# Kernel tuning notes

Hardware: AMD Instinct MI355X
Metric: run time of the kernel (lower is better)

The kernel has to match this reference:

```python
import jax, jax.numpy as jnp
import numpy as np

V, E, H = 50000, 256, 256   # vocab, emb_dim, hid_dim
R, S, W = 64, 32, 64        # reviews, sentences/review, words/sentence
UF = 20                     # user feature dim


def _bigru_last(x, wih, whh, bih, bhh):
    """Bidirectional GRU over x [B,T,D]; returns sum of final hidden states of
    the two directions, shape [B,H]. Params stacked over direction axis 0."""
    Hh = whh.shape[-1]

    def onedir(xd, wi, wh, bi, bh):
        gx = jnp.einsum('btd,gd->btg', xd, wi) + bi  # [B,T,3H] input gates precomputed

        def step(h, gxt):
            gh = h @ wh.T + bh
            r = jax.nn.sigmoid(gxt[:, :Hh] + gh[:, :Hh])
            z = jax.nn.sigmoid(gxt[:, Hh:2 * Hh] + gh[:, Hh:2 * Hh])
            n = jnp.tanh(gxt[:, 2 * Hh:] + r * gh[:, 2 * Hh:])
            return (1.0 - z) * n + z * h, None

        h0 = jnp.zeros((xd.shape[0], Hh), xd.dtype)
        hT, _ = jax.lax.scan(step, h0, jnp.swapaxes(gx, 0, 1))
        return hT

    return (onedir(x, wih[0], whh[0], bih[0], bhh[0])
            + onedir(x[:, ::-1], wih[1], whh[1], bih[1], bhh[1]))


def setup_inputs() -> dict:
    key = jax.random.key(0)
    ks = iter(jax.random.split(key, 40))

    def wmat(shape, scale=0.05):
        return jax.random.normal(next(ks), shape, jnp.float32) * scale

    inp = {}
    inp['inputs'] = jax.random.randint(next(ks), (R, S, W), 0, V)
    inp['sent_lengths'] = jax.random.randint(next(ks), (R, S), 1, W)
    inp['sent_counts'] = jax.random.randint(next(ks), (R,), 1, S)
    inp['user_feats'] = jax.random.normal(next(ks), (R, UF), jnp.float32)
    inp['embed'] = wmat((V, E))
    for name, din in (('wg', E), ('sg', H), ('rg', H + UF)):
        inp[name + '_wih'] = wmat((2, 3 * H, din))
        inp[name + '_whh'] = wmat((2, 3 * H, H))
        inp[name + '_bih'] = jnp.zeros((2, 3 * H), jnp.float32)
        inp[name + '_bhh'] = jnp.zeros((2, 3 * H), jnp.float32)
    inp['rfc_w1'] = wmat((H // 2, H + UF)); inp['rfc_b1'] = jnp.zeros((H // 2,), jnp.float32)
    inp['rfc_w2'] = wmat((1, H // 2));      inp['rfc_b2'] = jnp.zeros((1,), jnp.float32)
    inp['pfc_w1'] = wmat((H // 2, H));      inp['pfc_b1'] = jnp.zeros((H // 2,), jnp.float32)
    inp['pfc_w2'] = wmat((9, H // 2));      inp['pfc_b2'] = jnp.zeros((9,), jnp.float32)
    inp['uf_w'] = jnp.ones((UF,), jnp.float32)  # user_feats_weights
    return inp


def reference(inputs, sent_lengths, sent_counts, user_feats, embed,
              wg_wih, wg_whh, wg_bih, wg_bhh,
              sg_wih, sg_whh, sg_bih, sg_bhh,
              rg_wih, rg_whh, rg_bih, rg_bhh,
              rfc_w1, rfc_b1, rfc_w2, rfc_b2,
              pfc_w1, pfc_b1, pfc_w2, pfc_b2, uf_w):
    Rr, Sr, Wr = inputs.shape
    emb = embed[inputs]  # [R,S,W,E]  (dropout = identity in eval mode)
    # word-level bi-GRU, all R*S sentences batched together
    sent = _bigru_last(emb.reshape(Rr * Sr, Wr, emb.shape[-1]),
                       wg_wih, wg_whh, wg_bih, wg_bhh).reshape(Rr, Sr, -1)
    # sentence-level bi-GRU, batch over reviews
    rev = _bigru_last(sent, sg_wih, sg_whh, sg_bih, sg_bhh)  # [R,H]
    # F.normalize(user_feats) * user_feats_weights
    nrm = jnp.maximum(jnp.linalg.norm(user_feats, axis=-1, keepdims=True), 1e-12)
    p_batch = jnp.concatenate([rev, (user_feats / nrm) * uf_w], axis=-1)  # [R,H+20]
    r_stars = (jax.nn.selu(p_batch @ rfc_w1.T + rfc_b1) @ rfc_w2.T + rfc_b2)[:, 0]  # [R]
    # review-level bi-GRU over the sequence of reviews (batch 1)
    doc = _bigru_last(p_batch[None], rg_wih, rg_whh, rg_bih, rg_bhh)[0]  # [H]
    p_stars = jax.nn.selu(doc @ pfc_w1.T + pfc_b1) @ pfc_w2.T + pfc_b2  # [9]
    return p_stars, r_stars
```

## Files before the change

kernel.cpp:

```cpp
#include <hip/hip_runtime.h>
#include <math.h>

#define R_ 64
#define S_ 32
#define W_ 64
#define H_ 256
#define UF_ 20
#define TC 4

typedef short bf16x8 __attribute__((ext_vector_type(8)));
typedef float f32x4  __attribute__((ext_vector_type(4)));

#define MFMA(a,b,c) __builtin_amdgcn_mfma_f32_16x16x32_bf16((a),(b),(c),0,0,0)

typedef const unsigned int __attribute__((address_space(1)))* gp_t;
typedef unsigned int __attribute__((address_space(3)))* lp_t;
#define GLOAD16(SRC, DST) \
  __builtin_amdgcn_global_load_lds((gp_t)(const void*)(SRC), (lp_t)(void*)(DST), 16, 0, 0)

#define SW(r) ((((r)>>1)&7)<<3)

#define BFRAG(ff) ((ff) < 40 ? Breg[(ff) < 40 ? (ff) : 0] \
                 : *(const bf16x8*)&Bl[w][(ff) >= 40 ? (ff)-40 : 0][l*8])

__device__ __forceinline__ float sigf(float x){ return 1.0f/(1.0f+__expf(-x)); }
__device__ __forceinline__ float tanhf_(float x){ float e=__expf(2.0f*x); return 1.0f-2.0f/(e+1.0f); }
__device__ __forceinline__ float seluf_(float x){
  const float sc=1.0507009873554805f, al=1.6732632423543772f;
  return x>0.0f ? sc*x : sc*al*(expf(x)-1.0f);
}
__device__ __forceinline__ short tobf(float f){
  unsigned u=__float_as_uint(f); u += 0x7fffu + ((u>>16)&1u); return (short)(u>>16);
}
__device__ __forceinline__ float bf2f(short s){
  return __uint_as_float(((unsigned)(unsigned short)s) << 16);
}
__device__ __forceinline__ unsigned pk2(float a, float b){
  return (unsigned)(unsigned short)tobf(a) | ((unsigned)(unsigned short)tobf(b) << 16);
}

__global__ void prep_word_w(const float* __restrict__ wih, const float* __restrict__ whh,
                            short* __restrict__ Bw)
{
  int idx = blockIdx.x*256 + threadIdx.x;
  int lane = idx & 63;
  int rest = idx >> 6;
  int f  = rest % 6;  rest /= 6;
  int kt = rest % 16; rest /= 16;
  int w  = rest % 8;
  int d  = rest / 8;
  int gate = f >> 1;
  int j = 32*w + (f&1)*16 + (lane&15);
  int row = gate*256 + j;
  const float* W = (kt < 8 ? wih : whh) + (size_t)d*768*256;
  int k = (kt&7)*32 + (lane>>4)*8;
  short* dst = Bw + ((((size_t)(d*8 + w)*16 + kt)*6 + f)*64 + lane)*8;
#pragma unroll
  for (int jj=0;jj<8;jj++) dst[jj] = tobf(W[(size_t)row*256 + k + jj]);
}

__global__ void prep_rnn_w(const float* __restrict__ whh, short* __restrict__ Bs)
{
  int idx = blockIdx.x*256 + threadIdx.x;
  int lane = idx & 63;
  int rest = idx >> 6;
  int f  = rest % 6; rest /= 6;
  int kt = rest % 8; rest /= 8;
  int w  = rest % 8;
  int d  = rest / 8;
  int j = 32*w + (f&1)*16 + (lane&15);
  int row = (f>>1)*256 + j;
  const float* W = whh + (size_t)d*768*256;
  int k = kt*32 + (lane>>4)*8;
  short* dst = Bs + ((((size_t)(d*8 + w)*8 + kt)*6 + f)*64 + lane)*8;
#pragma unroll
  for (int jj=0;jj<8;jj++) dst[jj] = tobf(W[(size_t)row*256 + k + jj]);
}

__global__ void prep_gemm_w(const float* __restrict__ Wsrc, short* __restrict__ Bg)
{
  int idx = blockIdx.x*256 + threadIdx.x;
  int lane = idx & 63;
  int rest = idx >> 6;
  int kt = rest % 8;
  int nt = rest / 8;
  int n = nt*16 + (lane&15);
  int k = kt*32 + (lane>>4)*8;
  short* dst = Bg + (((size_t)nt*8 + kt)*64 + lane)*8;
#pragma unroll
  for (int jj=0;jj<8;jj++) dst[jj] = tobf(Wsrc[(size_t)n*256 + k + jj]);
}

__global__ __launch_bounds__(256) void gemm_gxu(
    const short* __restrict__ Ab, const float* __restrict__ Af,
    const int* __restrict__ toks, const short* __restrict__ Bg,
    const float* __restrict__ bih, const float* __restrict__ bhh,
    short* __restrict__ C, long Czoff,
    int mode, int t0, int Mclamp, int Cstride)
{
  const int z  = blockIdx.z;
  const int m0 = blockIdx.x * 64;
  const int yt = blockIdx.y * 8;
  const int ntb = (mode == 2 ? z*48 : 0) + yt;
  const int tid = threadIdx.x;
  const int w = tid >> 6, l = tid & 63;
  const int c = l & 15, q = l >> 4;
  __shared__ short As[64][264];
  {
    const int row = tid >> 2, c0 = (tid & 3) * 64;
    if (mode == 0) {
      const uint4* s = (const uint4*)(Ab + (size_t)(m0+row)*256 + c0);
#pragma unroll
      for (int i = 0; i < 8; i++) *(uint4*)&As[row][c0 + i*8] = s[i];
    } else {
      int r;
      if (mode == 1) {
        r = m0 + row; if (r >= Mclamp) r = Mclamp - 1;
      } else {
        const int rr = m0 + row;
        const int s_ = rr / TC, i_ = rr % TC;
        const int wd = z ? (63 - (t0 + i_)) : (t0 + i_);
        r = toks[s_*64 + wd];
      }
      const float* s = Af + (size_t)r*256 + c0;
#pragma unroll
      for (int i = 0; i < 8; i++) {
        float4 v0 = *(const float4*)(s + i*8);
        float4 v1 = *(const float4*)(s + i*8 + 4);
        uint4 u;
        u.x = pk2(v0.x, v0.y); u.y = pk2(v0.z, v0.w);
        u.z = pk2(v1.x, v1.y); u.w = pk2(v1.z, v1.w);
        *(uint4*)&As[row][c0 + i*8] = u;
      }
    }
  }
  float bias[2];
#pragma unroll
  for (int nt = 0; nt < 2; nt++) {
    const int coln = (yt + 2*w + nt)*16 + c;
    const int bidx = (mode == 2 ? z*768 : 0) + coln;
    bias[nt] = bih[bidx] + ((bidx % 768) < 512 ? bhh[bidx] : 0.0f);
  }
  __syncthreads();
  f32x4 acc[4][2];
#pragma unroll
  for (int a = 0; a < 4; a++) { acc[a][0] = (f32x4)0.f; acc[a][1] = (f32x4)0.f; }
#pragma unroll
  for (int kt = 0; kt < 8; kt++) {
    const int ko = kt*32 + q*8;
    bf16x8 a0 = *(const bf16x8*)&As[ 0+c][ko];
    bf16x8 a1 = *(const bf16x8*)&As[16+c][ko];
    bf16x8 a2 = *(const bf16x8*)&As[32+c][ko];
    bf16x8 a3 = *(const bf16x8*)&As[48+c][ko];
    bf16x8 b0 = *(const bf16x8*)&Bg[(((size_t)(ntb + 2*w    )*8 + kt)*64 + l)*8];
    bf16x8 b1 = *(const bf16x8*)&Bg[(((size_t)(ntb + 2*w + 1)*8 + kt)*64 + l)*8];
    acc[0][0]=MFMA(a0,b0,acc[0][0]); acc[1][0]=MFMA(a1,b0,acc[1][0]);
    acc[2][0]=MFMA(a2,b0,acc[2][0]); acc[3][0]=MFMA(a3,b0,acc[3][0]);
    acc[0][1]=MFMA(a0,b1,acc[0][1]); acc[1][1]=MFMA(a1,b1,acc[1][1]);
    acc[2][1]=MFMA(a2,b1,acc[2][1]); acc[3][1]=MFMA(a3,b1,acc[3][1]);
  }
  short* Cz = C + (size_t)z * Czoff;
#pragma unroll
  for (int mt = 0; mt < 4; mt++)
#pragma unroll
  for (int nt = 0; nt < 2; nt++)
#pragma unroll
  for (int rg = 0; rg < 4; rg++)
    Cz[(size_t)(m0 + mt*16 + q*4 + rg)*Cstride + (yt + 2*w + nt)*16 + c] =
        tobf(acc[mt][nt][rg] + bias[nt]);
}

__device__ __forceinline__ void stage_issue(
    short* dstbase,
    int mode, int d, int g, int w, int l,
    int nwords, int t0, int tt,
    const int* tokp, const short* gxF, const short* gxB)
{
  const char* bF = (const char*)gxF;
  const char* bB = (const char*)gxB;
#pragma unroll
  for (int i = 0; i < 3; i++) {
    const int off = i*1024 + l*16;
    const int rl  = (off >= 1536) ? 1 : 0;
    const int col = off - rl*1536;
    const char* src;
    if (mode == 0) {
      const int tx  = d ? (nwords - 1 - tt) : tt;
      const int tok = tokp[(2*w + rl)*64 + tx];
      src = bF + (size_t)tok*3072 + d*1536 + col;
    } else if (mode == 1) {
      const int ri = (g*16 + 2*w + rl)*TC + (tt - t0);
      src = (d ? bB : bF) + (size_t)ri*1536 + col;
    } else {
      const int se  = d ? (nwords - 1 - tt) : tt;
      const int row = g*16 + 2*w + rl;
      src = bF + ((size_t)row*nwords + se)*3072 + (size_t)d*1536 + col;
    }
    GLOAD16(src, dstbase + (size_t)w*1544 + i*512);
  }
}

__global__ __launch_bounds__(512, 2) void gru_rec(
    const int* __restrict__ toks,
    const short* __restrict__ gxF, const short* __restrict__ gxB,
    const short* __restrict__ Bh, int wstride, int koff,
    const float* __restrict__ bhh,
    float* __restrict__ hstate, int NS,
    int t0, int nsteps, int mode, int nwords)
{
  const int d = blockIdx.x & 1;
  const int g = blockIdx.x >> 1;
  const int tid = threadIdx.x;
  const int w = tid >> 6, l = tid & 63;
  const int c = l & 15, q = l >> 4;
  const int j0 = 32*w + c;

  __shared__ short gbuf[2][8][1544];
  __shared__ short hbf[2][16][256];
  __shared__ short Bl[8][8][512];
  __shared__ int   tokL[1024];

  if (mode == 0)
    for (int i = tid; i < 1024; i += 512) tokL[i] = toks[(size_t)g*1024 + i];

  bf16x8 Breg[40];
  {
    const short* Bb = Bh + (size_t)(d*8 + w)*wstride + (size_t)koff*3072 + l*8;
#pragma unroll
    for (int ff = 0; ff < 48; ff++) {
      bf16x8 v = *(const bf16x8*)(Bb + ff*512);
      if (ff < 40) Breg[ff] = v;
      else *(bf16x8*)&Bl[w][ff-40][l*8] = v;
    }
  }

  float bNH[2];
#pragma unroll
  for (int jt = 0; jt < 2; jt++)
    bNH[jt] = bhh[d*768 + 512 + j0 + jt*16];

  float hst[2][4];
  const int cur0 = t0 & 1;
  if (t0 == 0) {
#pragma unroll
    for (int a = 0; a < 2; a++)
#pragma unroll
    for (int r = 0; r < 4; r++) hst[a][r] = 0.0f;
  } else {
#pragma unroll
    for (int jt = 0; jt < 2; jt++)
#pragma unroll
    for (int rg = 0; rg < 4; rg++)
      hst[jt][rg] = hstate[((size_t)d*NS + g*16 + q*4 + rg)*256 + j0 + jt*16];
  }
#pragma unroll
  for (int jt = 0; jt < 2; jt++)
#pragma unroll
  for (int rg = 0; rg < 4; rg++) {
    const int m = q*4 + rg;
    hbf[cur0][m][(j0 + jt*16) ^ SW(m)] = tobf(hst[jt][rg]);
  }

  stage_issue(&gbuf[cur0][0][0], mode, d, g, w, l, nwords, t0, t0,
              (mode == 0) ? toks + (size_t)g*1024 : (const int*)nullptr, gxF, gxB);

  __syncthreads();

  const int tend = t0 + nsteps;
  for (int t = t0; t < tend; t++) {
    const int cur = t & 1, nxt = 1 - cur;

    if (t + 1 < tend)
      stage_issue(&gbuf[nxt][0][0], mode, d, g, w, l, nwords, t0, t + 1,
                  tokL, gxF, gxB);

    bf16x8 areg[8];
#pragma unroll
    for (int kt = 0; kt < 8; kt++)
      areg[kt] = *(const bf16x8*)&hbf[cur][c][(kt*32 + q*8) ^ SW(c)];

    short Gv[4][2][3];
#pragma unroll
    for (int rg = 0; rg < 4; rg++) {
      const int m = q*4 + rg;
      const short* gb = &gbuf[cur][0][0] + (m>>1)*1544 + (m&1)*768 + j0;
#pragma unroll
      for (int jt = 0; jt < 2; jt++)
#pragma unroll
      for (int ga = 0; ga < 3; ga++)
        Gv[rg][jt][ga] = gb[ga*256 + jt*16];
    }

    f32x4 accR[2], accZ[2], accNH[2];
#pragma unroll
    for (int a = 0; a < 2; a++) { accR[a]=(f32x4)0.f; accZ[a]=(f32x4)0.f; accNH[a]=(f32x4)0.f; }
#pragma unroll
    for (int kt = 0; kt < 8; kt++) {
      bf16x8 b0 = BFRAG(kt*6+0), b1 = BFRAG(kt*6+1),
             b2 = BFRAG(kt*6+2), b3 = BFRAG(kt*6+3);
      accR[0]=MFMA(areg[kt],b0,accR[0]);  accR[1]=MFMA(areg[kt],b1,accR[1]);
      accZ[0]=MFMA(areg[kt],b2,accZ[0]);  accZ[1]=MFMA(areg[kt],b3,accZ[1]);
    }
#pragma unroll
    for (int kt = 0; kt < 8; kt++) {
      bf16x8 b4 = BFRAG(kt*6+4), b5 = BFRAG(kt*6+5);
      accNH[0]=MFMA(areg[kt],b4,accNH[0]); accNH[1]=MFMA(areg[kt],b5,accNH[1]);
    }

    float rv[2][4], zv[2][4];
#pragma unroll
    for (int jt = 0; jt < 2; jt++)
#pragma unroll
    for (int rg = 0; rg < 4; rg++) {
      rv[jt][rg] = sigf(bf2f(Gv[rg][jt][0]) + accR[jt][rg]);
      zv[jt][rg] = sigf(bf2f(Gv[rg][jt][1]) + accZ[jt][rg]);
    }
#pragma unroll
    for (int jt = 0; jt < 2; jt++)
#pragma unroll
    for (int rg = 0; rg < 4; rg++) {
      const int m = q*4 + rg;
      const float n = tanhf_(bf2f(Gv[rg][jt][2]) + rv[jt][rg]*(accNH[jt][rg] + bNH[jt]));
      const float h = n + zv[jt][rg]*(hst[jt][rg] - n);
      hst[jt][rg] = h;
      hbf[nxt][m][(j0 + jt*16) ^ SW(m)] = tobf(h);
    }
    __syncthreads();
  }

#pragma unroll
  for (int jt = 0; jt < 2; jt++)
#pragma unroll
  for (int rg = 0; rg < 4; rg++)
    hstate[((size_t)d*NS + g*16 + q*4 + rg)*256 + j0 + jt*16] = hst[jt][rg];
}

__global__ void add2bf(const float* __restrict__ a, const float* __restrict__ b,
                       short* __restrict__ o)
{
  int i = (blockIdx.x*256 + threadIdx.x)*4;
  float4 x = *(const float4*)&a[i];
  float4 y = *(const float4*)&b[i];
  *(uint2*)&o[i] = make_uint2(pk2(x.x+y.x, x.y+y.y), pk2(x.z+y.z, x.w+y.w));
}

__global__ __launch_bounds__(512, 2) void rev_gru(
    const float* __restrict__ gx, const short* __restrict__ Br,
    const float* __restrict__ bhh,
    float* __restrict__ doc)
{
  const int d = blockIdx.x;
  const int tid = threadIdx.x;
  const int w = tid >> 6, l = tid & 63;
  const int c = l & 15, q = l >> 4;
  const int j0 = 32*w + c;

  __shared__ short hbf[2][16][256];
  __shared__ short Bl[8][8][512];
  for (int i = tid; i < 2*16*256; i += 512) ((short*)hbf)[i] = 0;

  bf16x8 Breg[40];
  {
    const short* Bbase = Br + (size_t)(d*8 + w)*8*6*512 + l*8;
#pragma unroll
    for (int ff = 0; ff < 48; ff++) {
      bf16x8 v = *(const bf16x8*)(Bbase + ff*512);
      if (ff < 40) Breg[ff] = v;
      else *(bf16x8*)&Bl[w][ff-40][l*8] = v;
    }
  }

  float bNH[2];
#pragma unroll
  for (int jt = 0; jt < 2; jt++)
    bNH[jt] = bhh[d*768 + 512 + j0 + jt*16];

  float hst[2];
  hst[0] = 0.0f; hst[1] = 0.0f;
  __syncthreads();

  for (int t = 0; t < 64; t++) {
    const int cur = t & 1, nxt = 1 - cur;
    const int teff = (d == 0) ? t : (63 - t);

    float G[2][3];
    if (q == 0) {
#pragma unroll
      for (int jt = 0; jt < 2; jt++) {
        const size_t row = (size_t)teff*1536 + d*768;
        const int j = j0 + jt*16;
        G[jt][0] = gx[row + j]; G[jt][1] = gx[row + 256 + j]; G[jt][2] = gx[row + 512 + j];
      }
    }

    bf16x8 areg[8];
#pragma unroll
    for (int kt = 0; kt < 8; kt++)
      areg[kt] = *(const bf16x8*)&hbf[cur][c][(kt*32 + q*8) ^ SW(c)];

    f32x4 accR[2], accZ[2], accNH[2];
#pragma unroll
    for (int a=0;a<2;a++) { accR[a]=(f32x4)0.f; accZ[a]=(f32x4)0.f; accNH[a]=(f32x4)0.f; }
#pragma unroll
    for (int kt = 0; kt < 8; kt++) {
      bf16x8 b0 = BFRAG(kt*6+0), b1 = BFRAG(kt*6+1),
             b2 = BFRAG(kt*6+2), b3 = BFRAG(kt*6+3);
      accR[0]=MFMA(areg[kt],b0,accR[0]);  accR[1]=MFMA(areg[kt],b1,accR[1]);
      accZ[0]=MFMA(areg[kt],b2,accZ[0]);  accZ[1]=MFMA(areg[kt],b3,accZ[1]);
    }
#pragma unroll
    for (int kt = 0; kt < 8; kt++) {
      bf16x8 b4 = BFRAG(kt*6+4), b5 = BFRAG(kt*6+5);
      accNH[0]=MFMA(areg[kt],b4,accNH[0]); accNH[1]=MFMA(areg[kt],b5,accNH[1]);
    }

    if (q == 0) {
#pragma unroll
      for (int jt = 0; jt < 2; jt++) {
        const float r = sigf(G[jt][0] + accR[jt][0]);
        const float z = sigf(G[jt][1] + accZ[jt][0]);
        const float n = tanhf_(G[jt][2] + r*(accNH[jt][0] + bNH[jt]));
        const float h = n + z*(hst[jt] - n);
        hst[jt] = h;
        hbf[nxt][0][j0 + jt*16] = tobf(h);
      }
    }
    __syncthreads();
  }
  if (q == 0) {
#pragma unroll
    for (int jt = 0; jt < 2; jt++)
      doc[d*256 + j0 + jt*16] = hst[jt];
  }
}

__global__ __launch_bounds__(256) void gemm_nt16(
    const float* __restrict__ A, const float* __restrict__ B,
    const float* __restrict__ bih, const float* __restrict__ bhh,
    float* __restrict__ C, int M, int N, int K)
{
  const int m0 = blockIdx.x * 16;
  const int n0 = blockIdx.y * 64;
  const int tid = threadIdx.x;
  __shared__ float As[16][17];
  __shared__ float Bs[16][68];
  float acc[4] = {0,0,0,0};
  const int m  = tid >> 4, n4 = (tid & 15) * 4;
  const int bn = tid >> 2, bk = (tid & 3) * 4;
  for (int k0 = 0; k0 < K; k0 += 16) {
    const int ak = tid & 15;
    float av = (k0 + ak < K) ? A[(size_t)(m0+m)*K + k0 + ak] : 0.0f;
    float4 b4 = make_float4(0,0,0,0);
    if (k0 + bk < K) b4 = *(const float4*)&B[(size_t)(n0+bn)*K + k0 + bk];
    __syncthreads();
    As[ak][m] = av;
    Bs[bk+0][bn]=b4.x; Bs[bk+1][bn]=b4.y; Bs[bk+2][bn]=b4.z; Bs[bk+3][bn]=b4.w;
    __syncthreads();
#pragma unroll
    for (int k = 0; k < 16; k++) {
      const float a = As[k][m];
      const float4 bb = *(const float4*)&Bs[k][n4];
      acc[0]+=a*bb.x; acc[1]+=a*bb.y; acc[2]+=a*bb.z; acc[3]+=a*bb.w;
    }
  }
#pragma unroll
  for (int i = 0; i < 4; i++) {
    const int n = n0 + n4 + i;
    acc[i] += bih[n] + ((n % 768) < 512 ? bhh[n] : 0.0f);
  }
  *(float4*)&C[(size_t)(m0+m)*N + n0+n4] = make_float4(acc[0],acc[1],acc[2],acc[3]);
}

__global__ void pbatch_k(const float* __restrict__ hs, const float* __restrict__ uf,
                         const float* __restrict__ ufw, float* __restrict__ pb)
{
  const int r = blockIdx.x, tid = threadIdx.x;
  __shared__ float nrm;
  if (tid == 0) {
    float s = 0.f;
    for (int i = 0; i < UF_; i++) { const float v = uf[r*UF_ + i]; s += v*v; }
    nrm = fmaxf(sqrtf(s), 1e-12f);
  }
  __syncthreads();
  if (tid < H_)  pb[r*276 + tid] = hs[r*H_ + tid] + hs[(size_t)R_*H_ + r*H_ + tid];
  if (tid < UF_) pb[r*276 + H_ + tid] = uf[r*UF_ + tid] / nrm * ufw[tid];
}

__global__ void rstars_k(const float* __restrict__ pb,
                         const float* __restrict__ w1, const float* __restrict__ b1,
                         const float* __restrict__ w2, const float* __restrict__ b2,
                         float* __restrict__ out)
{
  const int r = blockIdx.x, tid = threadIdx.x;
  __shared__ float ps[276];
  __shared__ float s1[128];
  for (int i = tid; i < 276; i += 128) ps[i] = pb[r*276 + i];
  __syncthreads();
  float a = b1[tid];
  for (int k = 0; k < 276; k++) a += ps[k] * w1[tid*276 + k];
  s1[tid] = seluf_(a);
  __syncthreads();
  if (tid == 0) {
    float s = b2[0];
    for (int k = 0; k < 128; k++) s += s1[k] * w2[k];
    out[9 + r] = s;
  }
}

__global__ void pstars_k(const float* __restrict__ doc2,
                         const float* __restrict__ w1, const float* __restrict__ b1,
                         const float* __restrict__ w2, const float* __restrict__ b2,
                         float* __restrict__ out)
{
  const int tid = threadIdx.x;
  __shared__ float dc[256];
  __shared__ float s1[128];
  dc[tid]       = doc2[tid];
  dc[128 + tid] = doc2[128 + tid];
  __syncthreads();
  float a = b1[tid];
  for (int k = 0; k < 256; k++) a += dc[k] * w1[tid*256 + k];
  s1[tid] = seluf_(a);
  __syncthreads();
  if (tid < 9) {
    float s = b2[tid];
    for (int k = 0; k < 128; k++) s += s1[k] * w2[tid*128 + k];
    out[tid] = s;
  }
}

__global__ void docsum_k(float* __restrict__ doc)
{
  const int tid = threadIdx.x;
  doc[tid] = doc[tid] + doc[256 + tid];
}

extern "C" void kernel_launch(void* const* d_in, const int* in_sizes, int n_in,
                              void* d_out, int out_size, void* d_ws, size_t ws_size,
                              hipStream_t stream)
{
  const int*   toks   = (const int*)  d_in[0];
  const float* uf     = (const float*)d_in[3];
  const float* embed  = (const float*)d_in[4];
  const float* wg_wih = (const float*)d_in[5];
  const float* wg_whh = (const float*)d_in[6];
  const float* wg_bih = (const float*)d_in[7];
  const float* wg_bhh = (const float*)d_in[8];
  const float* sg_wih = (const float*)d_in[9];
  const float* sg_whh = (const float*)d_in[10];
  const float* sg_bih = (const float*)d_in[11];
  const float* sg_bhh = (const float*)d_in[12];
  const float* rg_wih = (const float*)d_in[13];
  const float* rg_whh = (const float*)d_in[14];
  const float* rg_bih = (const float*)d_in[15];
  const float* rg_bhh = (const float*)d_in[16];
  const float* rfc_w1 = (const float*)d_in[17];
  const float* rfc_b1 = (const float*)d_in[18];
  const float* rfc_w2 = (const float*)d_in[19];
  const float* rfc_b2 = (const float*)d_in[20];
  const float* pfc_w1 = (const float*)d_in[21];
  const float* pfc_b1 = (const float*)d_in[22];
  const float* pfc_w2 = (const float*)d_in[23];
  const float* pfc_b2 = (const float*)d_in[24];
  const float* uf_w   = (const float*)d_in[25];
  float* out = (float*)d_out;
  float* ws  = (float*)d_ws;
  (void)in_sizes; (void)n_in; (void)out_size;

  const size_t OFF_BW   = 0;
  const size_t OFF_BS   = OFF_BW  + 393216;
  const size_t OFF_BR   = OFF_BS  + 196608;
  const size_t OFF_BG   = OFF_BR  + 196608;
  const size_t OFF_BGW  = OFF_BG  + 196608;
  const size_t OFF_HF   = OFF_BGW + 196608;
  const size_t OFF_SB   = OFF_HF  + 1048576;
  const size_t OFF_GXS  = OFF_SB  + 262144;
  const size_t OFF_HS   = OFF_GXS + 1572864;
  const size_t OFF_PB   = OFF_HS  + 32768;
  const size_t OFF_GXR  = OFF_PB  + 17664;
  const size_t OFF_DOC  = OFF_GXR + 98304;
  const size_t OFF_GXT  = OFF_DOC + 512;
  const size_t TOT_A    = OFF_GXT + (size_t)50048*1536/2;

  short* Bw   = (short*)(ws + OFF_BW);
  short* Bs   = (short*)(ws + OFF_BS);
  short* Br   = (short*)(ws + OFF_BR);
  short* Bg   = (short*)(ws + OFF_BG);
  short* Bgw  = (short*)(ws + OFF_BGW);
  float* hfin = ws + OFF_HF;
  short* sentb= (short*)(ws + OFF_SB);
  short* gxs  = (short*)(ws + OFF_GXS);
  float* hs   = ws + OFF_HS;
  float* pb   = ws + OFF_PB;
  float* gxr  = ws + OFF_GXR;
  float* doc  = ws + OFF_DOC;
  short* gxf  = (short*)(ws + OFF_GXT);
  short* gxb  = gxf + (size_t)8192*768;
  short* gxv  = (short*)(ws + OFF_GXT);

  const bool big = ws_size >= TOT_A * sizeof(float);

  prep_word_w<<<384, 256, 0, stream>>>(wg_wih, wg_whh, Bw);
  prep_rnn_w<<<192, 256, 0, stream>>>(sg_whh, Bs);
  prep_rnn_w<<<192, 256, 0, stream>>>(rg_whh, Br);
  prep_gemm_w<<<192, 256, 0, stream>>>(sg_wih, Bg);
  prep_gemm_w<<<192, 256, 0, stream>>>(wg_wih, Bgw);

  if (big) {
    gemm_gxu<<<dim3(782, 12, 1), 256, 0, stream>>>(
        nullptr, embed, nullptr, Bgw, wg_bih, wg_bhh, gxv, 0, 1, 0, 50000, 1536);
    gru_rec<<<256, 512, 0, stream>>>(toks, gxv, nullptr, Bw, 49152, 8,
        wg_bhh, hfin, 2048, 0, 64, 0, 64);
  } else {
    for (int tc = 0; tc < 64/TC; tc++) {
      gemm_gxu<<<dim3(128, 6, 2), 256, 0, stream>>>(
          nullptr, embed, toks, Bgw, wg_bih, wg_bhh, gxf, (long)8192*768, 2, tc*TC, 0, 768);
      gru_rec<<<256, 512, 0, stream>>>(toks, gxf, gxb, Bw, 49152, 8,
          wg_bhh, hfin, 2048, tc*TC, TC, 1, 64);
    }
  }
  add2bf<<<512, 256, 0, stream>>>(hfin, hfin + (size_t)2048*256, sentb);

  gemm_gxu<<<dim3(32, 12, 1), 256, 0, stream>>>(
      sentb, nullptr, nullptr, Bg, sg_bih, sg_bhh, gxs, 0, 0, 0, 2048, 1536);
  gru_rec<<<8, 512, 0, stream>>>(nullptr, gxs, nullptr, Bs, 24576, 0,
      sg_bhh, hs, 64, 0, 32, 2, 32);

  pbatch_k<<<R_, 256, 0, stream>>>(hs, uf, uf_w, pb);
  rstars_k<<<R_, 128, 0, stream>>>(pb, rfc_w1, rfc_b1, rfc_w2, rfc_b2, out);

  gemm_nt16<<<dim3(4, 24), 256, 0, stream>>>(pb, rg_wih, rg_bih, rg_bhh, gxr, 64, 1536, 276);
  rev_gru<<<2, 512, 0, stream>>>(gxr, Br, rg_bhh, doc);
  docsum_k<<<1, 256, 0, stream>>>(doc);
  pstars_k<<<1, 128, 0, stream>>>(doc, pfc_w1, pfc_b1, pfc_w2, pfc_b2, out);
}
```

Before: 753.9 us.

## Triple-buffer gate prefetch with partial vmcnt barriers in GRU recurrence

```diff
diff --git a/kernel.cpp b/kernel.cpp
--- a/kernel.cpp
+++ b/kernel.cpp
@@ -22,6 +22,19 @@
 
 #define BFRAG(ff) ((ff) < 40 ? Breg[(ff) < 40 ? (ff) : 0] \
                  : *(const bf16x8*)&Bl[w][(ff) >= 40 ? (ff)-40 : 0][l*8])
+
+__device__ __forceinline__ void pbar3(){
+  asm volatile("s_waitcnt vmcnt(3) lgkmcnt(0)" ::: "memory");
+  __builtin_amdgcn_sched_barrier(0);
+  __builtin_amdgcn_s_barrier();
+  __builtin_amdgcn_sched_barrier(0);
+}
+__device__ __forceinline__ void pbar0(){
+  asm volatile("s_waitcnt vmcnt(0) lgkmcnt(0)" ::: "memory");
+  __builtin_amdgcn_sched_barrier(0);
+  __builtin_amdgcn_s_barrier();
+  __builtin_amdgcn_sched_barrier(0);
+}
 
 __device__ __forceinline__ float sigf(float x){ return 1.0f/(1.0f+__expf(-x)); }
 __device__ __forceinline__ float tanhf_(float x){ float e=__expf(2.0f*x); return 1.0f-2.0f/(e+1.0f); }
@@ -174,7 +187,8 @@
     short* dstbase,
     int mode, int d, int g, int w, int l,
     int nwords, int t0, int tt,
-    const int* tokp, const short* gxF, const short* gxB)
+    const int* tokg, const unsigned short* tokl,
+    const short* gxF, const short* gxB)
 {
   const char* bF = (const char*)gxF;
   const char* bB = (const char*)gxB;
@@ -186,7 +200,8 @@
     const char* src;
     if (mode == 0) {
       const int tx  = d ? (nwords - 1 - tt) : tt;
-      const int tok = tokp[(2*w + rl)*64 + tx];
+      const int tok = tokl ? (int)tokl[(2*w + rl)*64 + tx]
+                           : tokg[(2*w + rl)*64 + tx];
       src = bF + (size_t)tok*3072 + d*1536 + col;
     } else if (mode == 1) {
       const int ri = (g*16 + 2*w + rl)*TC + (tt - t0);
@@ -215,13 +230,14 @@
   const int c = l & 15, q = l >> 4;
   const int j0 = 32*w + c;
 
-  __shared__ short gbuf[2][8][1544];
+  __shared__ short gbuf[3][8][1544];
   __shared__ short hbf[2][16][256];
   __shared__ short Bl[8][8][512];
-  __shared__ int   tokL[1024];
+  __shared__ unsigned short tokL[1024];
 
   if (mode == 0)
-    for (int i = tid; i < 1024; i += 512) tokL[i] = toks[(size_t)g*1024 + i];
+    for (int i = tid; i < 1024; i += 512)
+      tokL[i] = (unsigned short)toks[(size_t)g*1024 + i];
 
   bf16x8 Breg[40];
   {
@@ -261,35 +277,32 @@
     hbf[cur0][m][(j0 + jt*16) ^ SW(m)] = tobf(hst[jt][rg]);
   }
 
-  stage_issue(&gbuf[cur0][0][0], mode, d, g, w, l, nwords, t0, t0,
-              (mode == 0) ? toks + (size_t)g*1024 : (const int*)nullptr, gxF, gxB);
-
-  __syncthreads();
-
   const int tend = t0 + nsteps;
+  const int* tg = (mode == 0) ? toks + (size_t)g*1024 : (const int*)nullptr;
+
+  stage_issue(&gbuf[t0 % 3][0][0], mode, d, g, w, l, nwords, t0, t0,
+              tg, nullptr, gxF, gxB);
+  if (t0 + 1 < tend) {
+    stage_issue(&gbuf[(t0+1) % 3][0][0], mode, d, g, w, l, nwords, t0, t0 + 1,
+                tg, nullptr, gxF, gxB);
+    pbar3();
+  } else {
+    pbar0();
+  }
+
   for (int t = t0; t < tend; t++) {
     const int cur = t & 1, nxt = 1 - cur;
-
-    if (t + 1 < tend)
-      stage_issue(&gbuf[nxt][0][0], mode, d, g, w, l, nwords, t0, t + 1,
-                  tokL, gxF, gxB);
+    const int gcur = t % 3;
+
+    const bool more = (t + 2 < tend);
+    if (more)
+      stage_issue(&gbuf[(t+2) % 3][0][0], mode, d, g, w, l, nwords, t0, t + 2,
+                  nullptr, tokL, gxF, gxB);
 
     bf16x8 areg[8];
 #pragma unroll
     for (int kt = 0; kt < 8; kt++)
       areg[kt] = *(const bf16x8*)&hbf[cur][c][(kt*32 + q*8) ^ SW(c)];
-
-    short Gv[4][2][3];
-#pragma unroll
-    for (int rg = 0; rg < 4; rg++) {
-      const int m = q*4 + rg;
-      const short* gb = &gbuf[cur][0][0] + (m>>1)*1544 + (m&1)*768 + j0;
-#pragma unroll
-      for (int jt = 0; jt < 2; jt++)
-#pragma unroll
-      for (int ga = 0; ga < 3; ga++)
-        Gv[rg][jt][ga] = gb[ga*256 + jt*16];
-    }
 
     f32x4 accR[2], accZ[2], accNH[2];
 #pragma unroll
@@ -301,6 +314,19 @@
       accR[0]=MFMA(areg[kt],b0,accR[0]);  accR[1]=MFMA(areg[kt],b1,accR[1]);
       accZ[0]=MFMA(areg[kt],b2,accZ[0]);  accZ[1]=MFMA(areg[kt],b3,accZ[1]);
     }
+
+    short Gv[4][2][3];
+#pragma unroll
+    for (int rg = 0; rg < 4; rg++) {
+      const int m = q*4 + rg;
+      const short* gb = &gbuf[gcur][0][0] + (m>>1)*1544 + (m&1)*768 + j0;
+#pragma unroll
+      for (int jt = 0; jt < 2; jt++)
+#pragma unroll
+      for (int ga = 0; ga < 3; ga++)
+        Gv[rg][jt][ga] = gb[ga*256 + jt*16];
+    }
+
 #pragma unroll
     for (int kt = 0; kt < 8; kt++) {
       bf16x8 b4 = BFRAG(kt*6+4), b5 = BFRAG(kt*6+5);
@@ -325,7 +351,8 @@
       hst[jt][rg] = h;
       hbf[nxt][m][(j0 + jt*16) ^ SW(m)] = tobf(h);
     }
-    __syncthreads();
+
+    if (more) pbar3(); else pbar0();
   }
 
 #pragma unroll
```

Measured after the change: 774.7 us. 1.03x slower.
